# Performance work log

Hardware: AMD Instinct MI355X
Metric: run time of the kernel (lower is better)

Reference implementation:

```python
import jax, jax.numpy as jnp
import numpy as np

# Graph/block sizes: 2-hop sampled minibatch
N0, N1, N2 = 655360, 81920, 8192   # src nodes layer0, dst0/src1, dst1 (seeds)
FAN0, FAN1 = 8, 10
E0, E1 = N1 * FAN0, N2 * FAN1       # 655360, 81920
F_IN, H = 128, 256
BN_EPS = 1e-5
L2_EPS = 1e-12


def setup_inputs() -> dict:
    key = jax.random.key(0)
    ks = jax.random.split(key, 16)
    s = 0.05  # param scale
    inp = {
        "x": jax.random.normal(ks[0], (N0, F_IN), jnp.float32),
        "edge_src0": jax.random.randint(ks[1], (E0,), 0, N0, jnp.int32),
        "edge_dst0": jnp.repeat(jnp.arange(N1, dtype=jnp.int32), FAN0),
        "edge_src1": jax.random.randint(ks[2], (E1,), 0, N1, jnp.int32),
        "edge_dst1": jnp.repeat(jnp.arange(N2, dtype=jnp.int32), FAN1),
        "W_pool0": jax.random.normal(ks[3], (F_IN, F_IN), jnp.float32) * s,
        "b_pool0": jnp.zeros((F_IN,), jnp.float32),
        "W_self0": jax.random.normal(ks[4], (F_IN, H), jnp.float32) * s,
        "W_neigh0": jax.random.normal(ks[5], (F_IN, H), jnp.float32) * s,
        "b0": jnp.zeros((H,), jnp.float32),
        "W_pool1": jax.random.normal(ks[6], (H, H), jnp.float32) * s,
        "b_pool1": jnp.zeros((H,), jnp.float32),
        "W_self1": jax.random.normal(ks[7], (H, H), jnp.float32) * s,
        "W_neigh1": jax.random.normal(ks[8], (H, H), jnp.float32) * s,
        "b1": jnp.zeros((H,), jnp.float32),
        "g_bn0": jnp.ones((H,), jnp.float32),
        "be_bn0": jnp.zeros((H,), jnp.float32),
        "W_h": jax.random.normal(ks[9], (H, H), jnp.float32) * s,
        "b_h": jnp.zeros((H,), jnp.float32),
        "g_bnh": jnp.ones((H,), jnp.float32),
        "be_bnh": jnp.zeros((H,), jnp.float32),
        "W_lat": jax.random.normal(ks[10], (H, H), jnp.float32) * s,
        "b_lat": jnp.zeros((H,), jnp.float32),
        "g_bnl": jnp.ones((H,), jnp.float32),
        "be_bnl": jnp.zeros((H,), jnp.float32),
    }
    return inp


def _sage_pool(h, esrc, edst, n_dst, Wp, bp, Ws, Wn, b):
    # DGL SAGEConv aggregator_type='pool':
    # m = relu(fc_pool(h_src)); pooled[v] = max_{u in N(v)} m[u]
    # out = fc_self(h_dst) + fc_neigh(pooled) + bias
    m = jax.nn.relu(h @ Wp + bp)                                  # [N_src, d]
    pooled = jax.ops.segment_max(m[esrc], edst, num_segments=n_dst)
    return h[:n_dst] @ Ws + pooled @ Wn + b


def _l2norm(h):
    n = jnp.sqrt(jnp.sum(h * h, axis=1, keepdims=True))
    return h / jnp.maximum(n, L2_EPS)


def _bn(h, g, b):
    mu = jnp.mean(h, axis=0)
    var = jnp.var(h, axis=0)
    return (h - mu) * jax.lax.rsqrt(var + BN_EPS) * g + b


def reference(x, edge_src0, edge_dst0, edge_src1, edge_dst1,
              W_pool0, b_pool0, W_self0, W_neigh0, b0,
              W_pool1, b_pool1, W_self1, W_neigh1, b1,
              g_bn0, be_bn0, W_h, b_h, g_bnh, be_bnh,
              W_lat, b_lat, g_bnl, be_bnl):
    # layer 0
    h = _sage_pool(x, edge_src0, edge_dst0, N1, W_pool0, b_pool0, W_self0, W_neigh0, b0)
    h = _l2norm(h)
    h = jax.nn.relu(_bn(h, g_bn0, be_bn0))
    # dropout: eval mode (identity)
    h = jax.nn.relu(_bn(h @ W_h + b_h, g_bnh, be_bnh))   # self.hidden
    # layer 1 (last conv)
    h = _sage_pool(h, edge_src1, edge_dst1, N2, W_pool1, b_pool1, W_self1, W_neigh1, b1)
    h = _l2norm(h)
    # self.latent
    h = _bn(h @ W_lat + b_lat, g_bnl, be_bnl)
    return h
```

## Files before the change

### kernel.cpp

```cpp
#include <hip/hip_runtime.h>

typedef unsigned short u16;
typedef unsigned int u32;
typedef float f32x4 __attribute__((ext_vector_type(4)));
typedef int i32x4 __attribute__((ext_vector_type(4)));
typedef __bf16 bf16x8 __attribute__((ext_vector_type(8)));
typedef short s16x8 __attribute__((ext_vector_type(8)));

#define CN0 655360
#define CN1 81920
#define CN2 8192

#define H0_OFF    0ull
#define T_OFF     41943040ull
#define H2_OFF    83886080ull
#define ZZ_OFF    88080384ull
#define WP0F_OFF  96468992ull
#define WC0F_OFF  96501760ull
#define WHF_OFF   96632832ull
#define WP1F_OFF  96763904ull
#define WC1F_OFF  96894976ull
#define WLATF_OFF 97157120ull
#define STAT_OFF  97288192ull
#define SS_OFF    97294336ull

__device__ inline u16 f2bf(float f) {
  u32 u = __builtin_bit_cast(u32, f);
  return (u16)((u + 0x7fffu + ((u >> 16) & 1u)) >> 16);
}
__device__ inline float bf2f(u16 s) {
  return __builtin_bit_cast(float, (u32)s << 16);
}
__device__ inline i32x4 cvt8(f32x4 a, f32x4 b) {
  union { bf16x8 v; i32x4 q; } u;
  #pragma unroll
  for (int j = 0; j < 4; ++j) { u.v[j] = (__bf16)a[j]; u.v[4 + j] = (__bf16)b[j]; }
  return u.q;
}

template <typename V>
__device__ inline auto mfma_sel(V a, V b, f32x4 c, int)
    -> decltype(__builtin_amdgcn_mfma_f32_16x16x32_bf16(a, b, c, 0, 0, 0)) {
  return __builtin_amdgcn_mfma_f32_16x16x32_bf16(a, b, c, 0, 0, 0);
}
template <typename V>
__device__ inline f32x4 mfma_sel(V a, V b, f32x4 c, long) {
  return __builtin_amdgcn_mfma_f32_16x16x32_bf16(
      __builtin_bit_cast(s16x8, a), __builtin_bit_cast(s16x8, b), c, 0, 0, 0);
}
__device__ inline f32x4 MFMA(i32x4 a, i32x4 b, f32x4 c) {
  return mfma_sel(__builtin_bit_cast(bf16x8, a), __builtin_bit_cast(bf16x8, b), c, 0);
}

__device__ void fragify(const float* W0, const float* W1, int Khalf, int N,
                        u16* dst, int tid, int nthr) {
  int K = W1 ? 2 * Khalf : Khalf;
  int ntile = N >> 4;
  int total = (K >> 5) * ntile * 512;
  for (int i = tid; i < total; i += nthr) {
    int j = i & 7;
    int lane = (i >> 3) & 63;
    int nt = (i >> 9) % ntile;
    int kt = i / (512 * ntile);
    int k = kt * 32 + ((lane >> 4) << 3) + j;
    int n = nt * 16 + (lane & 15);
    float v = (k < Khalf) ? W0[k * N + n] : W1[(k - Khalf) * N + n];
    dst[i] = f2bf(v);
  }
}

__global__ void kprep(const float* Wp0, const float* Ws0, const float* Wn0,
                      const float* Wh, const float* Wp1, const float* Ws1,
                      const float* Wn1, const float* Wlat,
                      u16* wp0f, u16* wc0f, u16* whf, u16* wp1f, u16* wc1f,
                      u16* wlatf) {
  int tid = blockIdx.x * blockDim.x + threadIdx.x;
  int nthr = gridDim.x * blockDim.x;
  fragify(Wp0, nullptr, 128, 128, wp0f, tid, nthr);
  fragify(Ws0, Wn0, 128, 256, wc0f, tid, nthr);
  fragify(Wh, nullptr, 256, 256, whf, tid, nthr);
  fragify(Wp1, nullptr, 256, 256, wp1f, tid, nthr);
  fragify(Ws1, Wn1, 256, 256, wc1f, tid, nthr);
  fragify(Wlat, nullptr, 256, 256, wlatf, tid, nthr);
}

__global__ void kfin(const float* __restrict__ stat, float inv_n,
                     const float* __restrict__ g, const float* __restrict__ be,
                     float* __restrict__ ssout) {
  int c = threadIdx.x;
  float mu = stat[c] * inv_n;
  float var = stat[256 + c] * inv_n - mu * mu;
  float sc = g[c] / sqrtf(var + 1e-5f);
  ssout[c] = sc;
  ssout[256 + c] = be[c] - mu * sc;
}

__global__ __launch_bounds__(256, 3)
void k1_layer0(const float* __restrict__ x, const int* __restrict__ esrc,
               const u16* __restrict__ wp0f, const u16* __restrict__ wc0f,
               const float* __restrict__ bp0, const float* __restrict__ b0v,
               u16* __restrict__ h0, float* __restrict__ stat0) {
  __shared__ __align__(16) char lds[16896];
  float* rsb = (float*)(lds + 16384);
  int tid = threadIdx.x, lane = tid & 63, w = tid >> 6;
  int r15 = lane & 15, g = lane >> 4;
  int d0 = blockIdx.x * 32;

  {
    int e0 = d0 * 8 + w * 64;
    const float* rp[4];
    #pragma unroll
    for (int rt = 0; rt < 4; ++rt)
      rp[rt] = x + (size_t)esrc[e0 + rt * 16 + r15] * 128;
    i32x4 afr[4][4];
    #pragma unroll
    for (int rt = 0; rt < 4; ++rt)
      #pragma unroll
      for (int kt = 0; kt < 4; ++kt) {
        f32x4 p0 = *(const f32x4*)(rp[rt] + kt * 32 + g * 8);
        f32x4 p1 = *(const f32x4*)(rp[rt] + kt * 32 + g * 8 + 4);
        afr[rt][kt] = cvt8(p0, p1);
      }
    for (int nt = 0; nt < 8; ++nt) {
      f32x4 acc[4] = {};
      #pragma unroll
      for (int kt = 0; kt < 4; ++kt) {
        i32x4 b = *(const i32x4*)(wp0f + (((kt * 8 + nt) * 64 + lane) << 3));
        #pragma unroll
        for (int rt = 0; rt < 4; ++rt) acc[rt] = MFMA(afr[rt][kt], b, acc[rt]);
      }
      float bias = bp0[nt * 16 + r15];
      #pragma unroll
      for (int rt = 0; rt < 4; ++rt) {
        float mx = fmaxf(fmaxf(acc[rt][0], acc[rt][1]), fmaxf(acc[rt][2], acc[rt][3]));
        mx = fmaxf(mx + bias, 0.0f);
        mx = fmaxf(mx, __shfl_xor(mx, 16));
        if ((g & 1) == 0) {
          u32 row = (u32)(w * 8 + rt * 2 + (g >> 1));
          u32 byte = (row * 512 + 256 + (u32)(nt * 16 + r15) * 2) ^ ((row & 7) << 4);
          *(u16*)(lds + byte) = f2bf(mx);
        }
      }
    }
  }

  {
    int i = tid >> 3, part = tid & 7;
    const float* xr = x + (size_t)(d0 + i) * 128 + part * 16;
    f32x4 t0 = *(const f32x4*)(xr + 0);
    f32x4 t1 = *(const f32x4*)(xr + 4);
    f32x4 t2 = *(const f32x4*)(xr + 8);
    f32x4 t3 = *(const f32x4*)(xr + 12);
    u32 sw = (u32)((i & 7) << 4);
    *(i32x4*)(lds + (((u32)i * 512 + (u32)part * 32) ^ sw)) = cvt8(t0, t1);
    *(i32x4*)(lds + (((u32)i * 512 + (u32)part * 32 + 16) ^ sw)) = cvt8(t2, t3);
  }
  __syncthreads();

  f32x4 acc2[4][2] = {};
  for (int kt = 0; kt < 8; ++kt) {
    u32 r0 = (u32)r15, r1 = (u32)(16 + r15);
    i32x4 a0 = *(const i32x4*)(lds + ((r0 * 512 + (u32)kt * 64 + (u32)g * 16) ^ ((r0 & 7) << 4)));
    i32x4 a1 = *(const i32x4*)(lds + ((r1 * 512 + (u32)kt * 64 + (u32)g * 16) ^ ((r1 & 7) << 4)));
    #pragma unroll
    for (int n4 = 0; n4 < 4; ++n4) {
      int nt = w * 4 + n4;
      i32x4 b = *(const i32x4*)(wc0f + (((size_t)(kt * 16 + nt) * 64 + lane) << 3));
      acc2[n4][0] = MFMA(a0, b, acc2[n4][0]);
      acc2[n4][1] = MFMA(a1, b, acc2[n4][1]);
    }
  }

  float vn[4][2][4];
  #pragma unroll
  for (int n4 = 0; n4 < 4; ++n4) {
    float bv = b0v[(w * 4 + n4) * 16 + r15];
    #pragma unroll
    for (int rt = 0; rt < 2; ++rt)
      #pragma unroll
      for (int j = 0; j < 4; ++j) vn[n4][rt][j] = acc2[n4][rt][j] + bv;
  }
  float ssq[2][4];
  #pragma unroll
  for (int rt = 0; rt < 2; ++rt)
    #pragma unroll
    for (int j = 0; j < 4; ++j) {
      float s = 0.0f;
      #pragma unroll
      for (int n4 = 0; n4 < 4; ++n4) s += vn[n4][rt][j] * vn[n4][rt][j];
      s += __shfl_xor(s, 1); s += __shfl_xor(s, 2);
      s += __shfl_xor(s, 4); s += __shfl_xor(s, 8);
      ssq[rt][j] = s;
      if (r15 == 0) rsb[(rt * 16 + g * 4 + j) * 4 + w] = s;
    }
  __syncthreads();

  #pragma unroll
  for (int rt = 0; rt < 2; ++rt)
    #pragma unroll
    for (int j = 0; j < 4; ++j) {
      int r = rt * 16 + g * 4 + j;
      f32x4 q = *(const f32x4*)&rsb[r * 4];
      float rn = 1.0f / fmaxf(sqrtf(q[0] + q[1] + q[2] + q[3]), 1e-12f);
      #pragma unroll
      for (int n4 = 0; n4 < 4; ++n4) vn[n4][rt][j] *= rn;
    }
  #pragma unroll
  for (int n4 = 0; n4 < 4; ++n4) {
    int col = (w * 4 + n4) * 16 + r15;
    float s1 = 0.0f, s2 = 0.0f;
    #pragma unroll
    for (int rt = 0; rt < 2; ++rt)
      #pragma unroll
      for (int j = 0; j < 4; ++j) { float v = vn[n4][rt][j]; s1 += v; s2 += v * v; }
    s1 += __shfl_xor(s1, 16); s1 += __shfl_xor(s1, 32);
    s2 += __shfl_xor(s2, 16); s2 += __shfl_xor(s2, 32);
    if (g == 0) { atomicAdd(&stat0[col], s1); atomicAdd(&stat0[256 + col], s2); }
  }
  #pragma unroll
  for (int n4 = 0; n4 < 4; ++n4)
    #pragma unroll
    for (int rt = 0; rt < 2; ++rt)
      #pragma unroll
      for (int j = 0; j < 4; ++j)
        *(u16*)(lds + (u32)(rt * 16 + g * 4 + j) * 512 + (u32)((w * 4 + n4) * 16 + r15) * 2)
            = f2bf(vn[n4][rt][j]);
  __syncthreads();
  {
    int i = tid >> 3, c8 = tid & 7;
    const char* srcp = lds + i * 512 + c8 * 64;
    u16* dst = h0 + (size_t)(d0 + i) * 256 + c8 * 32;
    #pragma unroll
    for (int c = 0; c < 4; ++c)
      *(i32x4*)(dst + c * 8) = *(const i32x4*)(srcp + c * 16);
  }
}

template <bool RELU_OUT, bool STATS, bool H2OUT>
__global__ __launch_bounds__(256, 4)
void gemm64(const u16* __restrict__ Ain, const float* __restrict__ ss,
            const u16* __restrict__ Bf, const float* __restrict__ bias,
            u16* __restrict__ Out, float* __restrict__ stat,
            u16* __restrict__ H2out) {
  __shared__ __align__(16) char lds[34816];
  u16* tb = (u16*)lds;
  float* scs = (float*)(lds + 32768);
  int tid = threadIdx.x, lane = tid & 63, w = tid >> 6;
  int r15 = lane & 15, g = lane >> 4;
  int d0 = blockIdx.x * 64;
  scs[tid] = ss[tid];
  scs[256 + tid] = ss[256 + tid];
  __syncthreads();

  {
    int i = tid >> 2, part = tid & 3;
    const u16* ar = Ain + (size_t)(d0 + i) * 256 + part * 64;
    u32 sw = (u32)((i & 7) << 4), rowb = (u32)i * 512;
    for (int cc = 0; cc < 8; ++cc) {
      union { i32x4 q; u16 h[8]; } in, out;
      in.q = *(const i32x4*)(ar + cc * 8);
      #pragma unroll
      for (int j = 0; j < 8; ++j) {
        int k = part * 64 + cc * 8 + j;
        float v = fmaxf(bf2f(in.h[j]) * scs[k] + scs[256 + k], 0.0f);
        out.h[j] = f2bf(v);
      }
      *(i32x4*)(lds + ((rowb + (u32)(part * 64 + cc * 8) * 2) ^ sw)) = out.q;
    }
  }
  __syncthreads();

  f32x4 acc[4][4] = {};
  for (int kt = 0; kt < 8; ++kt) {
    i32x4 a[4];
    #pragma unroll
    for (int rt = 0; rt < 4; ++rt) {
      u32 r = (u32)(rt * 16 + r15);
      a[rt] = *(const i32x4*)(lds + ((r * 512 + (u32)kt * 64 + (u32)g * 16) ^ ((r & 7) << 4)));
    }
    #pragma unroll
    for (int n4 = 0; n4 < 4; ++n4) {
      int nt = w * 4 + n4;
      i32x4 b = *(const i32x4*)(Bf + (((size_t)(kt * 16 + nt) * 64 + lane) << 3));
      #pragma unroll
      for (int rt = 0; rt < 4; ++rt) acc[n4][rt] = MFMA(a[rt], b, acc[n4][rt]);
    }
  }
  __syncthreads();

  if constexpr (H2OUT) {
    if (d0 < CN2) {
      int i = tid >> 2, part = tid & 3;
      u16* orow = H2out + (size_t)(d0 + i) * 256 + part * 64;
      u32 sw = (u32)((i & 7) << 4);
      #pragma unroll
      for (int cc = 0; cc < 8; ++cc)
        *(i32x4*)(orow + cc * 8) =
            *(const i32x4*)(lds + (((u32)i * 512 + (u32)(part * 64 + cc * 8) * 2) ^ sw));
    }
    __syncthreads();
  }

  #pragma unroll
  for (int n4 = 0; n4 < 4; ++n4) {
    int col = (w * 4 + n4) * 16 + r15;
    float bv = bias[col];
    #pragma unroll
    for (int rt = 0; rt < 4; ++rt)
      #pragma unroll
      for (int j = 0; j < 4; ++j) {
        float v = acc[n4][rt][j] + bv;
        if (RELU_OUT) v = fmaxf(v, 0.0f);
        tb[(rt * 16 + g * 4 + j) * 256 + col] = f2bf(v);
      }
  }
  __syncthreads();

  {
    int i = tid >> 2, part = tid & 3;
    u16* orow = Out + (size_t)(d0 + i) * 256 + part * 64;
    const u16* trow = tb + i * 256 + part * 64;
    #pragma unroll
    for (int cc = 0; cc < 8; ++cc)
      *(i32x4*)(orow + cc * 8) = *(const i32x4*)(trow + cc * 8);
  }
  if (STATS) {
    int c = tid; float s1 = 0.0f, s2 = 0.0f;
    for (int r = 0; r < 64; ++r) { float v = bf2f(tb[r * 256 + c]); s1 += v; s2 += v * v; }
    atomicAdd(&stat[c], s1); atomicAdd(&stat[256 + c], s2);
  }
}

__global__ __launch_bounds__(256, 2)
void k6_layer1(const int* __restrict__ esrc1, const u16* __restrict__ m1,
               const u16* __restrict__ h2, const u16* __restrict__ wc1f,
               const u16* __restrict__ wlatf, const float* __restrict__ b1v,
               const float* __restrict__ blat, float* __restrict__ zz,
               float* __restrict__ statl) {
  __shared__ __align__(16) char lds[81920];
  float* zbuf = (float*)(lds + 32768);
  int tid = threadIdx.x, lane = tid & 63, w = tid >> 6;
  int r15 = lane & 15, g = lane >> 4;
  int d0 = blockIdx.x * 32;

  {
    int i = tid >> 3, part = tid & 7;
    u32 sw = (u32)((i & 7) << 4);
    const u16* hrow = h2 + (size_t)(d0 + i) * 256 + part * 32;
    #pragma unroll
    for (int cc = 0; cc < 4; ++cc) {
      i32x4 q = *(const i32x4*)(hrow + cc * 8);
      *(i32x4*)(lds + (((u32)i * 1024 + (u32)(part * 32 + cc * 8) * 2) ^ sw)) = q;
    }
    float mx[32];
    #pragma unroll
    for (int c = 0; c < 32; ++c) mx[c] = -1e30f;
    for (int e = 0; e < 10; ++e) {
      int src = esrc1[(d0 + i) * 10 + e];
      const u16* mrow = m1 + (size_t)src * 256 + part * 32;
      #pragma unroll
      for (int cc = 0; cc < 4; ++cc) {
        union { i32x4 q; u16 h[8]; } pk;
        pk.q = *(const i32x4*)(mrow + cc * 8);
        #pragma unroll
        for (int j = 0; j < 8; ++j) mx[cc * 8 + j] = fmaxf(mx[cc * 8 + j], bf2f(pk.h[j]));
      }
    }
    #pragma unroll
    for (int cc = 0; cc < 4; ++cc) {
      union { i32x4 q; u16 h[8]; } pk;
      #pragma unroll
      for (int j = 0; j < 8; ++j) pk.h[j] = f2bf(mx[cc * 8 + j]);
      *(i32x4*)(lds + (((u32)i * 1024 + (u32)(256 + part * 32 + cc * 8) * 2) ^ sw)) = pk.q;
    }
  }
  __syncthreads();

  {
    f32x4 acc[4][2] = {};
    for (int kt = 0; kt < 16; ++kt) {
      u32 r0 = (u32)r15, r1 = (u32)(16 + r15);
      i32x4 a0 = *(const i32x4*)(lds + ((r0 * 1024 + (u32)kt * 64 + (u32)g * 16) ^ ((r0 & 7) << 4)));
      i32x4 a1 = *(const i32x4*)(lds + ((r1 * 1024 + (u32)kt * 64 + (u32)g * 16) ^ ((r1 & 7) << 4)));
      #pragma unroll
      for (int n4 = 0; n4 < 4; ++n4) {
        int nt = w * 4 + n4;
        i32x4 b = *(const i32x4*)(wc1f + (((size_t)(kt * 16 + nt) * 64 + lane) << 3));
        acc[n4][0] = MFMA(a0, b, acc[n4][0]);
        acc[n4][1] = MFMA(a1, b, acc[n4][1]);
      }
    }
    #pragma unroll
    for (int n4 = 0; n4 < 4; ++n4) {
      int col = (w * 4 + n4) * 16 + r15;
      float bv = b1v[col];
      #pragma unroll
      for (int rt = 0; rt < 2; ++rt)
        #pragma unroll
        for (int j = 0; j < 4; ++j)
          zbuf[(rt * 16 + g * 4 + j) * 256 + col] = acc[n4][rt][j] + bv;
    }
  }
  __syncthreads();

  {
    int i = tid >> 3, part = tid & 7;
    float* zr = zbuf + i * 256 + part * 32;
    float v[32]; float ss = 0.0f;
    #pragma unroll
    for (int c = 0; c < 32; ++c) { v[c] = zr[c]; ss += v[c] * v[c]; }
    ss += __shfl_xor(ss, 1); ss += __shfl_xor(ss, 2); ss += __shfl_xor(ss, 4);
    float rn = 1.0f / fmaxf(sqrtf(ss), 1e-12f);
    u32 sw = (u32)((i & 7) << 4);
    #pragma unroll
    for (int cc = 0; cc < 4; ++cc) {
      union { i32x4 q; u16 h[8]; } pk;
      #pragma unroll
      for (int j = 0; j < 8; ++j) pk.h[j] = f2bf(v[cc * 8 + j] * rn);
      *(i32x4*)(lds + 65536 + (((u32)i * 512 + (u32)(part * 32 + cc * 8) * 2) ^ sw)) = pk.q;
    }
  }
  __syncthreads();

  {
    f32x4 acc[4][2] = {};
    for (int kt = 0; kt < 8; ++kt) {
      u32 r0 = (u32)r15, r1 = (u32)(16 + r15);
      i32x4 a0 = *(const i32x4*)(lds + 65536 + ((r0 * 512 + (u32)kt * 64 + (u32)g * 16) ^ ((r0 & 7) << 4)));
      i32x4 a1 = *(const i32x4*)(lds + 65536 + ((r1 * 512 + (u32)kt * 64 + (u32)g * 16) ^ ((r1 & 7) << 4)));
      #pragma unroll
      for (int n4 = 0; n4 < 4; ++n4) {
        int nt = w * 4 + n4;
        i32x4 b = *(const i32x4*)(wlatf + (((size_t)(kt * 16 + nt) * 64 + lane) << 3));
        acc[n4][0] = MFMA(a0, b, acc[n4][0]);
        acc[n4][1] = MFMA(a1, b, acc[n4][1]);
      }
    }
    #pragma unroll
    for (int n4 = 0; n4 < 4; ++n4) {
      int col = (w * 4 + n4) * 16 + r15;
      float bv = blat[col];
      #pragma unroll
      for (int rt = 0; rt < 2; ++rt)
        #pragma unroll
        for (int j = 0; j < 4; ++j)
          zbuf[(rt * 16 + g * 4 + j) * 256 + col] = acc[n4][rt][j] + bv;
    }
  }
  __syncthreads();

  {
    int i = tid >> 3, part = tid & 7;
    float* zr = zbuf + i * 256 + part * 32;
    float* orow = zz + (size_t)(d0 + i) * 256 + part * 32;
    #pragma unroll
    for (int c = 0; c < 32; c += 4) *(f32x4*)(orow + c) = *(const f32x4*)(zr + c);
  }
  {
    int c = tid; float s1 = 0.0f, s2 = 0.0f;
    for (int r = 0; r < 32; ++r) { float v = zbuf[r * 256 + c]; s1 += v; s2 += v * v; }
    atomicAdd(&statl[c], s1); atomicAdd(&statl[256 + c], s2);
  }
}

__global__ void k7_out(const float* __restrict__ zz, const float* __restrict__ ssl,
                       float* __restrict__ out) {
  int idx = blockIdx.x * 256 + threadIdx.x;
  int e0 = idx * 4;
  int c = e0 & 255;
  f32x4 v = *(const f32x4*)(zz + e0);
  f32x4 sc = *(const f32x4*)(ssl + c);
  f32x4 sh = *(const f32x4*)(ssl + 256 + c);
  *(f32x4*)(out + e0) = v * sc + sh;
}

extern "C" void kernel_launch(void* const* d_in, const int* in_sizes, int n_in,
                              void* d_out, int out_size, void* d_ws, size_t ws_size,
                              hipStream_t stream) {
  const float* x     = (const float*)d_in[0];
  const int*   es0   = (const int*)d_in[1];
  const int*   es1   = (const int*)d_in[3];
  const float* Wp0   = (const float*)d_in[5];
  const float* bp0   = (const float*)d_in[6];
  const float* Ws0   = (const float*)d_in[7];
  const float* Wn0   = (const float*)d_in[8];
  const float* b0v   = (const float*)d_in[9];
  const float* Wp1   = (const float*)d_in[10];
  const float* bp1   = (const float*)d_in[11];
  const float* Ws1   = (const float*)d_in[12];
  const float* Wn1   = (const float*)d_in[13];
  const float* b1v   = (const float*)d_in[14];
  const float* gbn0  = (const float*)d_in[15];
  const float* bebn0 = (const float*)d_in[16];
  const float* Wh    = (const float*)d_in[17];
  const float* bh    = (const float*)d_in[18];
  const float* gbnh  = (const float*)d_in[19];
  const float* bebnh = (const float*)d_in[20];
  const float* Wlat  = (const float*)d_in[21];
  const float* blat  = (const float*)d_in[22];
  const float* gbnl  = (const float*)d_in[23];
  const float* bebnl = (const float*)d_in[24];

  char* ws = (char*)d_ws;
  u16* h0    = (u16*)(ws + H0_OFF);
  u16* tban  = (u16*)(ws + T_OFF);
  u16* m1    = (u16*)(ws + H0_OFF);
  u16* h2    = (u16*)(ws + H2_OFF);
  float* zz  = (float*)(ws + ZZ_OFF);
  u16* wp0f  = (u16*)(ws + WP0F_OFF);
  u16* wc0f  = (u16*)(ws + WC0F_OFF);
  u16* whf   = (u16*)(ws + WHF_OFF);
  u16* wp1f  = (u16*)(ws + WP1F_OFF);
  u16* wc1f  = (u16*)(ws + WC1F_OFF);
  u16* wlatf = (u16*)(ws + WLATF_OFF);
  float* stat = (float*)(ws + STAT_OFF);
  float* ssv  = (float*)(ws + SS_OFF);

  hipMemsetAsync(stat, 0, 6 * 256 * sizeof(float), stream);
  kprep<<<64, 256, 0, stream>>>(Wp0, Ws0, Wn0, Wh, Wp1, Ws1, Wn1, Wlat,
                                wp0f, wc0f, whf, wp1f, wc1f, wlatf);
  k1_layer0<<<CN1 / 32, 256, 0, stream>>>(x, es0, wp0f, wc0f, bp0, b0v, h0, stat);
  kfin<<<1, 256, 0, stream>>>(stat, 1.0f / CN1, gbn0, bebn0, ssv);
  gemm64<false, true, false><<<CN1 / 64, 256, 0, stream>>>(h0, ssv, whf, bh, tban,
                                                           stat + 512, nullptr);
  kfin<<<1, 256, 0, stream>>>(stat + 512, 1.0f / CN1, gbnh, bebnh, ssv + 512);
  gemm64<true, false, true><<<CN1 / 64, 256, 0, stream>>>(tban, ssv + 512, wp1f, bp1,
                                                          m1, nullptr, h2);
  k6_layer1<<<CN2 / 32, 256, 0, stream>>>(es1, m1, h2, wc1f, wlatf, b1v, blat, zz,
                                          stat + 1024);
  kfin<<<1, 256, 0, stream>>>(stat + 1024, 1.0f / CN2, gbnl, bebnl, ssv + 1024);
  k7_out<<<out_size / 1024, 256, 0, stream>>>(zz, ssv + 1024, (float*)d_out);
  (void)in_sizes; (void)n_in; (void)ws_size;
}
```

Measured before the change: 283.4 us.

## Fold BN finalize into consumers, drop memset, shrink layer1 tiles, raise occupancy

Removes the three single-block kfin launches and the memset: the BN scale/shift is now computed inside the consuming gemm64/k7_out kernels, and the stats are zeroed inside kprep. k6_layer1 processes 16 rows per block instead of 32, halving its LDS so more blocks fit and the grid doubles. k1_layer0's launch bound rises to 4 blocks per SM, and its self-row x loads are issued before the gather phase. The aim is to cut launch gaps and improve latency hiding, at the cost of each block redundantly recomputing the BN coefficients and possible register pressure.

New measurement: 299.5 us. +5.7%, slower.

```diff
diff --git a/kernel.cpp b/kernel.cpp
--- a/kernel.cpp
+++ b/kernel.cpp
@@ -22,7 +22,6 @@
 #define WC1F_OFF  96894976ull
 #define WLATF_OFF 97157120ull
 #define STAT_OFF  97288192ull
-#define SS_OFF    97294336ull
 
 __device__ inline u16 f2bf(float f) {
   u32 u = __builtin_bit_cast(u32, f);
@@ -73,9 +72,13 @@
                       const float* Wh, const float* Wp1, const float* Ws1,
                       const float* Wn1, const float* Wlat,
                       u16* wp0f, u16* wc0f, u16* whf, u16* wp1f, u16* wc1f,
-                      u16* wlatf) {
+                      u16* wlatf, float* stat) {
   int tid = blockIdx.x * blockDim.x + threadIdx.x;
   int nthr = gridDim.x * blockDim.x;
+  if (blockIdx.x == 0) {
+    #pragma unroll
+    for (int i = 0; i < 6; ++i) stat[threadIdx.x + i * 256] = 0.0f;
+  }
   fragify(Wp0, nullptr, 128, 128, wp0f, tid, nthr);
   fragify(Ws0, Wn0, 128, 256, wc0f, tid, nthr);
   fragify(Wh, nullptr, 256, 256, whf, tid, nthr);
@@ -84,18 +87,7 @@
   fragify(Wlat, nullptr, 256, 256, wlatf, tid, nthr);
 }
 
-__global__ void kfin(const float* __restrict__ stat, float inv_n,
-                     const float* __restrict__ g, const float* __restrict__ be,
-                     float* __restrict__ ssout) {
-  int c = threadIdx.x;
-  float mu = stat[c] * inv_n;
-  float var = stat[256 + c] * inv_n - mu * mu;
-  float sc = g[c] / sqrtf(var + 1e-5f);
-  ssout[c] = sc;
-  ssout[256 + c] = be[c] - mu * sc;
-}
-
-__global__ __launch_bounds__(256, 3)
+__global__ __launch_bounds__(256, 4)
 void k1_layer0(const float* __restrict__ x, const int* __restrict__ esrc,
                const u16* __restrict__ wp0f, const u16* __restrict__ wc0f,
                const float* __restrict__ bp0, const float* __restrict__ b0v,
@@ -106,6 +98,13 @@
   int r15 = lane & 15, g = lane >> 4;
   int d0 = blockIdx.x * 32;
 
+  int i_ = tid >> 3, part_ = tid & 7;
+  const float* xr_ = x + (size_t)(d0 + i_) * 128 + part_ * 16;
+  f32x4 t0 = *(const f32x4*)(xr_ + 0);
+  f32x4 t1 = *(const f32x4*)(xr_ + 4);
+  f32x4 t2 = *(const f32x4*)(xr_ + 8);
+  f32x4 t3 = *(const f32x4*)(xr_ + 12);
+
   {
     int e0 = d0 * 8 + w * 64;
     const float* rp[4];
@@ -145,15 +144,9 @@
   }
 
   {
-    int i = tid >> 3, part = tid & 7;
-    const float* xr = x + (size_t)(d0 + i) * 128 + part * 16;
-    f32x4 t0 = *(const f32x4*)(xr + 0);
-    f32x4 t1 = *(const f32x4*)(xr + 4);
-    f32x4 t2 = *(const f32x4*)(xr + 8);
-    f32x4 t3 = *(const f32x4*)(xr + 12);
-    u32 sw = (u32)((i & 7) << 4);
-    *(i32x4*)(lds + (((u32)i * 512 + (u32)part * 32) ^ sw)) = cvt8(t0, t1);
-    *(i32x4*)(lds + (((u32)i * 512 + (u32)part * 32 + 16) ^ sw)) = cvt8(t2, t3);
+    u32 sw = (u32)((i_ & 7) << 4);
+    *(i32x4*)(lds + (((u32)i_ * 512 + (u32)part_ * 32) ^ sw)) = cvt8(t0, t1);
+    *(i32x4*)(lds + (((u32)i_ * 512 + (u32)part_ * 32 + 16) ^ sw)) = cvt8(t2, t3);
   }
   __syncthreads();
 
@@ -180,7 +173,6 @@
       #pragma unroll
       for (int j = 0; j < 4; ++j) vn[n4][rt][j] = acc2[n4][rt][j] + bv;
   }
-  float ssq[2][4];
   #pragma unroll
   for (int rt = 0; rt < 2; ++rt)
     #pragma unroll
@@ -190,7 +182,6 @@
       for (int n4 = 0; n4 < 4; ++n4) s += vn[n4][rt][j] * vn[n4][rt][j];
       s += __shfl_xor(s, 1); s += __shfl_xor(s, 2);
       s += __shfl_xor(s, 4); s += __shfl_xor(s, 8);
-      ssq[rt][j] = s;
       if (r15 == 0) rsb[(rt * 16 + g * 4 + j) * 4 + w] = s;
     }
   __syncthreads();
@@ -238,9 +229,10 @@
 
 template <bool RELU_OUT, bool STATS, bool H2OUT>
 __global__ __launch_bounds__(256, 4)
-void gemm64(const u16* __restrict__ Ain, const float* __restrict__ ss,
+void gemm64(const u16* __restrict__ Ain, const float* __restrict__ statin,
+            float inv_n, const float* __restrict__ gg, const float* __restrict__ bb,
             const u16* __restrict__ Bf, const float* __restrict__ bias,
-            u16* __restrict__ Out, float* __restrict__ stat,
+            u16* __restrict__ Out, float* __restrict__ statout,
             u16* __restrict__ H2out) {
   __shared__ __align__(16) char lds[34816];
   u16* tb = (u16*)lds;
@@ -248,8 +240,13 @@
   int tid = threadIdx.x, lane = tid & 63, w = tid >> 6;
   int r15 = lane & 15, g = lane >> 4;
   int d0 = blockIdx.x * 64;
-  scs[tid] = ss[tid];
-  scs[256 + tid] = ss[256 + tid];
+  {
+    float mu = statin[tid] * inv_n;
+    float var = statin[256 + tid] * inv_n - mu * mu;
+    float sc = gg[tid] / sqrtf(var + 1e-5f);
+    scs[tid] = sc;
+    scs[256 + tid] = bb[tid] - mu * sc;
+  }
   __syncthreads();
 
   {
@@ -327,67 +324,65 @@
   if (STATS) {
     int c = tid; float s1 = 0.0f, s2 = 0.0f;
     for (int r = 0; r < 64; ++r) { float v = bf2f(tb[r * 256 + c]); s1 += v; s2 += v * v; }
-    atomicAdd(&stat[c], s1); atomicAdd(&stat[256 + c], s2);
-  }
-}
-
-__global__ __launch_bounds__(256, 2)
+    atomicAdd(&statout[c], s1); atomicAdd(&statout[256 + c], s2);
+  }
+}
+
+__global__ __launch_bounds__(256, 4)
 void k6_layer1(const int* __restrict__ esrc1, const u16* __restrict__ m1,
                const u16* __restrict__ h2, const u16* __restrict__ wc1f,
                const u16* __restrict__ wlatf, const float* __restrict__ b1v,
                const float* __restrict__ blat, float* __restrict__ zz,
                float* __restrict__ statl) {
-  __shared__ __align__(16) char lds[81920];
-  float* zbuf = (float*)(lds + 32768);
+  __shared__ __align__(16) char lds[40960];
+  float* zbuf = (float*)(lds + 16384);
   int tid = threadIdx.x, lane = tid & 63, w = tid >> 6;
   int r15 = lane & 15, g = lane >> 4;
-  int d0 = blockIdx.x * 32;
-
-  {
-    int i = tid >> 3, part = tid & 7;
+  int d0 = blockIdx.x * 16;
+
+  {
+    int i = tid >> 4, part = tid & 15;
     u32 sw = (u32)((i & 7) << 4);
-    const u16* hrow = h2 + (size_t)(d0 + i) * 256 + part * 32;
-    #pragma unroll
-    for (int cc = 0; cc < 4; ++cc) {
-      i32x4 q = *(const i32x4*)(hrow + cc * 8);
-      *(i32x4*)(lds + (((u32)i * 1024 + (u32)(part * 32 + cc * 8) * 2) ^ sw)) = q;
-    }
-    float mx[32];
-    #pragma unroll
-    for (int c = 0; c < 32; ++c) mx[c] = -1e30f;
+    const u16* hrow = h2 + (size_t)(d0 + i) * 256 + part * 16;
+    i32x4 q0 = *(const i32x4*)(hrow);
+    i32x4 q1 = *(const i32x4*)(hrow + 8);
+    *(i32x4*)(lds + (((u32)i * 1024 + (u32)(part * 16) * 2) ^ sw)) = q0;
+    *(i32x4*)(lds + (((u32)i * 1024 + (u32)(part * 16) * 2 + 16) ^ sw)) = q1;
+    float mx[16];
+    #pragma unroll
+    for (int c = 0; c < 16; ++c) mx[c] = -1e30f;
+    const int* ep = esrc1 + (d0 + i) * 10;
+    #pragma unroll 2
     for (int e = 0; e < 10; ++e) {
-      int src = esrc1[(d0 + i) * 10 + e];
-      const u16* mrow = m1 + (size_t)src * 256 + part * 32;
-      #pragma unroll
-      for (int cc = 0; cc < 4; ++cc) {
-        union { i32x4 q; u16 h[8]; } pk;
-        pk.q = *(const i32x4*)(mrow + cc * 8);
-        #pragma unroll
-        for (int j = 0; j < 8; ++j) mx[cc * 8 + j] = fmaxf(mx[cc * 8 + j], bf2f(pk.h[j]));
-      }
-    }
-    #pragma unroll
-    for (int cc = 0; cc < 4; ++cc) {
-      union { i32x4 q; u16 h[8]; } pk;
-      #pragma unroll
-      for (int j = 0; j < 8; ++j) pk.h[j] = f2bf(mx[cc * 8 + j]);
-      *(i32x4*)(lds + (((u32)i * 1024 + (u32)(256 + part * 32 + cc * 8) * 2) ^ sw)) = pk.q;
-    }
-  }
-  __syncthreads();
-
-  {
-    f32x4 acc[4][2] = {};
+      int src = ep[e];
+      const u16* mrow = m1 + (size_t)src * 256 + part * 16;
+      union { i32x4 q; u16 h[8]; } a, b;
+      a.q = *(const i32x4*)(mrow);
+      b.q = *(const i32x4*)(mrow + 8);
+      #pragma unroll
+      for (int j = 0; j < 8; ++j) {
+        mx[j] = fmaxf(mx[j], bf2f(a.h[j]));
+        mx[8 + j] = fmaxf(mx[8 + j], bf2f(b.h[j]));
+      }
+    }
+    union { i32x4 q; u16 h[8]; } p0, p1;
+    #pragma unroll
+    for (int j = 0; j < 8; ++j) { p0.h[j] = f2bf(mx[j]); p1.h[j] = f2bf(mx[8 + j]); }
+    *(i32x4*)(lds + (((u32)i * 1024 + (u32)(256 + part * 16) * 2) ^ sw)) = p0.q;
+    *(i32x4*)(lds + (((u32)i * 1024 + (u32)(256 + part * 16) * 2 + 16) ^ sw)) = p1.q;
+  }
+  __syncthreads();
+
+  {
+    f32x4 acc[4] = {};
     for (int kt = 0; kt < 16; ++kt) {
-      u32 r0 = (u32)r15, r1 = (u32)(16 + r15);
+      u32 r0 = (u32)r15;
       i32x4 a0 = *(const i32x4*)(lds + ((r0 * 1024 + (u32)kt * 64 + (u32)g * 16) ^ ((r0 & 7) << 4)));
-      i32x4 a1 = *(const i32x4*)(lds + ((r1 * 1024 + (u32)kt * 64 + (u32)g * 16) ^ ((r1 & 7) << 4)));
       #pragma unroll
       for (int n4 = 0; n4 < 4; ++n4) {
         int nt = w * 4 + n4;
         i32x4 b = *(const i32x4*)(wc1f + (((size_t)(kt * 16 + nt) * 64 + lane) << 3));
-        acc[n4][0] = MFMA(a0, b, acc[n4][0]);
-        acc[n4][1] = MFMA(a1, b, acc[n4][1]);
+        acc[n4] = MFMA(a0, b, acc[n4]);
       }
     }
     #pragma unroll
@@ -395,45 +390,40 @@
       int col = (w * 4 + n4) * 16 + r15;
       float bv = b1v[col];
       #pragma unroll
-      for (int rt = 0; rt < 2; ++rt)
-        #pragma unroll
-        for (int j = 0; j < 4; ++j)
-          zbuf[(rt * 16 + g * 4 + j) * 256 + col] = acc[n4][rt][j] + bv;
-    }
-  }
-  __syncthreads();
-
-  {
-    int i = tid >> 3, part = tid & 7;
-    float* zr = zbuf + i * 256 + part * 32;
-    float v[32]; float ss = 0.0f;
-    #pragma unroll
-    for (int c = 0; c < 32; ++c) { v[c] = zr[c]; ss += v[c] * v[c]; }
-    ss += __shfl_xor(ss, 1); ss += __shfl_xor(ss, 2); ss += __shfl_xor(ss, 4);
+      for (int j = 0; j < 4; ++j)
+        zbuf[(g * 4 + j) * 256 + col] = acc[n4][j] + bv;
+    }
+  }
+  __syncthreads();
+
+  {
+    int i = tid >> 4, part = tid & 15;
+    float* zr = zbuf + i * 256 + part * 16;
+    f32x4 v0 = *(const f32x4*)(zr + 0), v1 = *(const f32x4*)(zr + 4);
+    f32x4 v2 = *(const f32x4*)(zr + 8), v3 = *(const f32x4*)(zr + 12);
+    float ss = 0.0f;
+    #pragma unroll
+    for (int j = 0; j < 4; ++j) ss += v0[j]*v0[j] + v1[j]*v1[j] + v2[j]*v2[j] + v3[j]*v3[j];
+    ss += __shfl_xor(ss, 1); ss += __shfl_xor(ss, 2);
+    ss += __shfl_xor(ss, 4); ss += __shfl_xor(ss, 8);
     float rn = 1.0f / fmaxf(sqrtf(ss), 1e-12f);
+    v0 *= rn; v1 *= rn; v2 *= rn; v3 *= rn;
     u32 sw = (u32)((i & 7) << 4);
-    #pragma unroll
-    for (int cc = 0; cc < 4; ++cc) {
-      union { i32x4 q; u16 h[8]; } pk;
-      #pragma unroll
-      for (int j = 0; j < 8; ++j) pk.h[j] = f2bf(v[cc * 8 + j] * rn);
-      *(i32x4*)(lds + 65536 + (((u32)i * 512 + (u32)(part * 32 + cc * 8) * 2) ^ sw)) = pk.q;
-    }
-  }
-  __syncthreads();
-
-  {
-    f32x4 acc[4][2] = {};
+    *(i32x4*)(lds + 32768 + (((u32)i * 512 + (u32)(part * 16) * 2) ^ sw)) = cvt8(v0, v1);
+    *(i32x4*)(lds + 32768 + (((u32)i * 512 + (u32)(part * 16) * 2 + 16) ^ sw)) = cvt8(v2, v3);
+  }
+  __syncthreads();
+
+  {
+    f32x4 acc[4] = {};
     for (int kt = 0; kt < 8; ++kt) {
-      u32 r0 = (u32)r15, r1 = (u32)(16 + r15);
-      i32x4 a0 = *(const i32x4*)(lds + 65536 + ((r0 * 512 + (u32)kt * 64 + (u32)g * 16) ^ ((r0 & 7) << 4)));
-      i32x4 a1 = *(const i32x4*)(lds + 65536 + ((r1 * 512 + (u32)kt * 64 + (u32)g * 16) ^ ((r1 & 7) << 4)));
+      u32 r0 = (u32)r15;
+      i32x4 a0 = *(const i32x4*)(lds + 32768 + ((r0 * 512 + (u32)kt * 64 + (u32)g * 16) ^ ((r0 & 7) << 4)));
       #pragma unroll
       for (int n4 = 0; n4 < 4; ++n4) {
         int nt = w * 4 + n4;
         i32x4 b = *(const i32x4*)(wlatf + (((size_t)(kt * 16 + nt) * 64 + lane) << 3));
-        acc[n4][0] = MFMA(a0, b, acc[n4][0]);
-        acc[n4][1] = MFMA(a1, b, acc[n4][1]);
+        acc[n4] = MFMA(a0, b, acc[n4]);
       }
     }
     #pragma unroll
@@ -441,37 +431,48 @@
       int col = (w * 4 + n4) * 16 + r15;
       float bv = blat[col];
       #pragma unroll
-      for (int rt = 0; rt < 2; ++rt)
-        #pragma unroll
-        for (int j = 0; j < 4; ++j)
-          zbuf[(rt * 16 + g * 4 + j) * 256 + col] = acc[n4][rt][j] + bv;
-    }
-  }
-  __syncthreads();
-
-  {
-    int i = tid >> 3, part = tid & 7;
-    float* zr = zbuf + i * 256 + part * 32;
-    float* orow = zz + (size_t)(d0 + i) * 256 + part * 32;
-    #pragma unroll
-    for (int c = 0; c < 32; c += 4) *(f32x4*)(orow + c) = *(const f32x4*)(zr + c);
+      for (int j = 0; j < 4; ++j)
+        zbuf[(g * 4 + j) * 256 + col] = acc[n4][j] + bv;
+    }
+  }
+  __syncthreads();
+
+  {
+    int i = tid >> 4, part = tid & 15;
+    float* zr = zbuf + i * 256 + part * 16;
+    float* orow = zz + (size_t)(d0 + i) * 256 + part * 16;
+    #pragma unroll
+    for (int c = 0; c < 16; c += 4) *(f32x4*)(orow + c) = *(const f32x4*)(zr + c);
   }
   {
     int c = tid; float s1 = 0.0f, s2 = 0.0f;
-    for (int r = 0; r < 32; ++r) { float v = zbuf[r * 256 + c]; s1 += v; s2 += v * v; }
+    #pragma unroll
+    for (int r = 0; r < 16; ++r) { float v = zbuf[r * 256 + c]; s1 += v; s2 += v * v; }
     atomicAdd(&statl[c], s1); atomicAdd(&statl[256 + c], s2);
   }
 }
 
-__global__ void k7_out(const float* __restrict__ zz, const float* __restrict__ ssl,
+__global__ void k7_out(const float* __restrict__ zz, const float* __restrict__ statl,
+                       const float* __restrict__ gg, const float* __restrict__ bb,
                        float* __restrict__ out) {
   int idx = blockIdx.x * 256 + threadIdx.x;
   int e0 = idx * 4;
   int c = e0 & 255;
+  const float inv_n = 1.0f / (float)CN2;
+  f32x4 s1 = *(const f32x4*)(statl + c);
+  f32x4 s2 = *(const f32x4*)(statl + 256 + c);
+  f32x4 gv = *(const f32x4*)(gg + c);
+  f32x4 bv = *(const f32x4*)(bb + c);
   f32x4 v = *(const f32x4*)(zz + e0);
-  f32x4 sc = *(const f32x4*)(ssl + c);
-  f32x4 sh = *(const f32x4*)(ssl + 256 + c);
-  *(f32x4*)(out + e0) = v * sc + sh;
+  f32x4 o;
+  #pragma unroll
+  for (int j = 0; j < 4; ++j) {
+    float mu = s1[j] * inv_n;
+    float var = s2[j] * inv_n - mu * mu;
+    float sc = gv[j] / sqrtf(var + 1e-5f);
+    o[j] = v[j] * sc + (bv[j] - mu * sc);
+  }
+  *(f32x4*)(out + e0) = o;
 }
 
 extern "C" void kernel_launch(void* const* d_in, const int* in_sizes, int n_in,
@@ -514,21 +515,17 @@
   u16* wc1f  = (u16*)(ws + WC1F_OFF);
   u16* wlatf = (u16*)(ws + WLATF_OFF);
   float* stat = (float*)(ws + STAT_OFF);
-  float* ssv  = (float*)(ws + SS_OFF);
-
-  hipMemsetAsync(stat, 0, 6 * 256 * sizeof(float), stream);
+
   kprep<<<64, 256, 0, stream>>>(Wp0, Ws0, Wn0, Wh, Wp1, Ws1, Wn1, Wlat,
-                                wp0f, wc0f, whf, wp1f, wc1f, wlatf);
+                                wp0f, wc0f, whf, wp1f, wc1f, wlatf, stat);
   k1_layer0<<<CN1 / 32, 256, 0, stream>>>(x, es0, wp0f, wc0f, bp0, b0v, h0, stat);
-  kfin<<<1, 256, 0, stream>>>(stat, 1.0f / CN1, gbn0, bebn0, ssv);
-  gemm64<false, true, false><<<CN1 / 64, 256, 0, stream>>>(h0, ssv, whf, bh, tban,
-                                                           stat + 512, nullptr);
-  kfin<<<1, 256, 0, stream>>>(stat + 512, 1.0f / CN1, gbnh, bebnh, ssv + 512);
-  gemm64<true, false, true><<<CN1 / 64, 256, 0, stream>>>(tban, ssv + 512, wp1f, bp1,
-                                                          m1, nullptr, h2);
-  k6_layer1<<<CN2 / 32, 256, 0, stream>>>(es1, m1, h2, wc1f, wlatf, b1v, blat, zz,
+  gemm64<false, true, false><<<CN1 / 64, 256, 0, stream>>>(
+      h0, stat, 1.0f / CN1, gbn0, bebn0, whf, bh, tban, stat + 512, nullptr);
+  gemm64<true, false, true><<<CN1 / 64, 256, 0, stream>>>(
+      tban, stat + 512, 1.0f / CN1, gbnh, bebnh, wp1f, bp1, m1, nullptr, h2);
+  k6_layer1<<<CN2 / 16, 256, 0, stream>>>(es1, m1, h2, wc1f, wlatf, b1v, blat, zz,
                                           stat + 1024);
-  kfin<<<1, 256, 0, stream>>>(stat + 1024, 1.0f / CN2, gbnl, bebnl, ssv + 1024);
-  k7_out<<<out_size / 1024, 256, 0, stream>>>(zz, ssv + 1024, (float*)d_out);
+  k7_out<<<out_size / 1024, 256, 0, stream>>>(zz, stat + 1024, gbnl, bebnl,
+                                              (float*)d_out);
   (void)in_sizes; (void)n_in; (void)ws_size;
 }
```
